# Kernel tuning notes

Hardware: AMD Instinct MI355X
Metric: run time of the kernel (lower is better)

The kernel has to match this reference:

```python
import jax, jax.numpy as jnp
import numpy as np

B, L, D = 32, 2048, 1024


def setup_inputs() -> dict:
    key = jax.random.key(0)
    ks = jax.random.split(key, 8)
    s = 1.0 / np.sqrt(D)
    s2 = 1.0 / np.sqrt(2 * D)
    return {
        "query": jax.random.normal(ks[0], (B, 1, D), dtype=jnp.float32),
        "context": jax.random.normal(ks[1], (B, L, D), dtype=jnp.float32),
        "W_in": jax.random.uniform(ks[2], (D, D), jnp.float32, -s, s),      # linear_in weight (no bias)
        "w_att": jax.random.uniform(ks[3], (2 * D,), jnp.float32, -s2, s2),  # nn.Linear(2D,1) weight, flattened
        "b_att": jax.random.uniform(ks[4], (1,), jnp.float32, -s2, s2),     # nn.Linear(2D,1) bias
        "W_out": jax.random.uniform(ks[5], (D, 2 * D), jnp.float32, -s2, s2),  # linear_out weight (no bias)
        "mask": jax.random.randint(ks[6], (B, L), 0, 2, dtype=jnp.int32),
    }


def reference(query, context, W_in, w_att, b_att, W_out, mask):
    # query: [B,1,D], context: [B,L,D], mask: [B,L]
    d = query.shape[-1]
    q = jnp.einsum('bd,ed->be', query[:, 0, :], W_in)  # linear_in: x @ W_in^T -> [B,D]
    # Additive score: tanh(Linear(cat([q_expanded, context])))
    # Split the [1, 2D] linear into query part and context part (no concat materialized).
    q_part = q @ w_att[:d]                               # [B]
    c_part = jnp.einsum('bld,d->bl', context, w_att[d:])  # [B,L]
    scores = jnp.tanh(q_part[:, None] + c_part + b_att[0])  # [B,L]
    scores = jnp.where(mask == 0, jnp.float32(-1e9), scores)
    weights = jax.nn.softmax(scores, axis=-1)            # [B,L]
    mix = jnp.einsum('bl,bld->bd', weights, context)     # [B,D]
    combined = jnp.concatenate([mix, q], axis=-1)        # [B,2D]
    output = jnp.tanh(combined @ W_out.T)[:, None, :]    # [B,1,D]
    return output, weights[:, None, :]
```

## Files before the change

### kernel.cpp

```cpp
#include <hip/hip_runtime.h>
#include <math.h>

#define B_DIM 32
#define L_DIM 2048
#define D_DIM 1024
#define NC    32
#define CHUNK (L_DIM / NC)
#define ROWS_PER_WAVE (CHUNK / 4)

__device__ __forceinline__ float wave_reduce_sum(float v) {
    #pragma unroll
    for (int off = 32; off > 0; off >>= 1)
        v += __shfl_xor(v, off, 64);
    return v;
}

__global__ __launch_bounds__(256) void k_linear_in(
        const float* __restrict__ query, const float* __restrict__ W_in,
        float* __restrict__ q_out) {
    const int wave = threadIdx.x >> 6;
    const int lane = threadIdx.x & 63;
    const int e = blockIdx.x * 4 + wave;
    const float4* W4 = (const float4*)(W_in + (size_t)e * D_DIM);
    float4 wrow[4];
    #pragma unroll
    for (int j = 0; j < 4; ++j) wrow[j] = W4[j * 64 + lane];
    for (int b = 0; b < B_DIM; ++b) {
        const float4* q4 = (const float4*)(query + (size_t)b * D_DIM);
        float local = 0.f;
        #pragma unroll
        for (int j = 0; j < 4; ++j) {
            float4 v = q4[j * 64 + lane];
            local += v.x * wrow[j].x + v.y * wrow[j].y
                   + v.z * wrow[j].z + v.w * wrow[j].w;
        }
        float s = wave_reduce_sum(local);
        if (lane == 0) q_out[(size_t)b * D_DIM + e] = s;
    }
}

__global__ __launch_bounds__(64) void k_spart(
        const float* __restrict__ q, const float* __restrict__ w_att,
        const float* __restrict__ b_att, float* __restrict__ spart) {
    const int b = blockIdx.x;
    const int lane = threadIdx.x;
    const float4* q4 = (const float4*)(q + (size_t)b * D_DIM);
    const float4* w4 = (const float4*)(w_att);
    float local = 0.f;
    #pragma unroll
    for (int j = 0; j < 4; ++j) {
        float4 a = q4[j * 64 + lane];
        float4 w = w4[j * 64 + lane];
        local += a.x * w.x + a.y * w.y + a.z * w.z + a.w * w.w;
    }
    float s = wave_reduce_sum(local);
    if (lane == 0) spart[b] = s + b_att[0];
}

__global__ __launch_bounds__(256) void k_scores(
        const float* __restrict__ context, const float* __restrict__ w_att,
        const int* __restrict__ mask, const float* __restrict__ spart,
        float* __restrict__ out_weights,
        float* __restrict__ pZ, float* __restrict__ pacc) {
    const int c = blockIdx.x;
    const int b = blockIdx.y;
    const int wave = threadIdx.x >> 6;
    const int lane = threadIdx.x & 63;

    float4 wc[4];
    const float4* w4 = (const float4*)(w_att + D_DIM);
    #pragma unroll
    for (int j = 0; j < 4; ++j) wc[j] = w4[j * 64 + lane];

    const float sp = spart[b];
    float4 acc[4];
    #pragma unroll
    for (int j = 0; j < 4; ++j) acc[j] = make_float4(0.f, 0.f, 0.f, 0.f);
    float z = 0.f;

    const int l0 = c * CHUNK;
    const float* ctx_b = context + (size_t)b * L_DIM * D_DIM;
    const int* mask_b = mask + (size_t)b * L_DIM;

    for (int r = 0; r < ROWS_PER_WAVE; ++r) {
        const int l = l0 + r * 4 + wave;
        const float4* row4 = (const float4*)(ctx_b + (size_t)l * D_DIM);
        float4 v[4];
        #pragma unroll
        for (int j = 0; j < 4; ++j) v[j] = row4[j * 64 + lane];
        float local = 0.f;
        #pragma unroll
        for (int j = 0; j < 4; ++j)
            local += v[j].x * wc[j].x + v[j].y * wc[j].y
                   + v[j].z * wc[j].z + v[j].w * wc[j].w;
        float s = wave_reduce_sum(local);
        float w = (mask_b[l] == 0) ? 0.f : expf(tanhf(sp + s));
        if (lane == 0) out_weights[(size_t)b * L_DIM + l] = w;
        z += w;
        #pragma unroll
        for (int j = 0; j < 4; ++j) {
            acc[j].x += w * v[j].x;
            acc[j].y += w * v[j].y;
            acc[j].z += w * v[j].z;
            acc[j].w += w * v[j].w;
        }
    }

    __shared__ float sacc[4][D_DIM];
    __shared__ float sz[4];
    #pragma unroll
    for (int j = 0; j < 4; ++j)
        ((float4*)sacc[wave])[j * 64 + lane] = acc[j];
    if (lane == 0) sz[wave] = z;
    __syncthreads();

    const int t = threadIdx.x;
    float4 s0 = ((const float4*)sacc[0])[t];
    float4 s1 = ((const float4*)sacc[1])[t];
    float4 s2 = ((const float4*)sacc[2])[t];
    float4 s3 = ((const float4*)sacc[3])[t];
    float4 tot;
    tot.x = s0.x + s1.x + s2.x + s3.x;
    tot.y = s0.y + s1.y + s2.y + s3.y;
    tot.z = s0.z + s1.z + s2.z + s3.z;
    tot.w = s0.w + s1.w + s2.w + s3.w;
    ((float4*)(pacc + ((size_t)(b * NC + c)) * D_DIM))[t] = tot;
    if (t == 0) pZ[b * NC + c] = sz[0] + sz[1] + sz[2] + sz[3];
}

__global__ __launch_bounds__(256) void k_reduce(
        const float* __restrict__ pacc, const float* __restrict__ pZ,
        float* __restrict__ mix, float* __restrict__ out_weights) {
    const int b = blockIdx.x;
    const int t = threadIdx.x;
    __shared__ float sInvZ;
    if (t == 0) {
        float zt = 0.f;
        for (int c = 0; c < NC; ++c) zt += pZ[b * NC + c];
        sInvZ = (zt > 0.f) ? 1.f / zt : 0.f;
    }
    __syncthreads();
    const float invZ = sInvZ;

    float4 tot = make_float4(0.f, 0.f, 0.f, 0.f);
    for (int c = 0; c < NC; ++c) {
        float4 v = ((const float4*)(pacc + ((size_t)(b * NC + c)) * D_DIM))[t];
        tot.x += v.x; tot.y += v.y; tot.z += v.z; tot.w += v.w;
    }
    tot.x *= invZ; tot.y *= invZ; tot.z *= invZ; tot.w *= invZ;
    ((float4*)(mix + (size_t)b * D_DIM))[t] = tot;

    #pragma unroll
    for (int i = 0; i < L_DIM / 256; ++i) {
        const size_t idx = (size_t)b * L_DIM + i * 256 + t;
        out_weights[idx] = out_weights[idx] * invZ;
    }
}

__global__ __launch_bounds__(256) void k_out(
        const float* __restrict__ mix, const float* __restrict__ q,
        const float* __restrict__ W_out, float* __restrict__ out) {
    const int wave = threadIdx.x >> 6;
    const int lane = threadIdx.x & 63;
    const int e = blockIdx.x * 4 + wave;
    const float4* W4 = (const float4*)(W_out + (size_t)e * (2 * D_DIM));
    float4 wrow[8];
    #pragma unroll
    for (int j = 0; j < 8; ++j) wrow[j] = W4[j * 64 + lane];
    for (int b = 0; b < B_DIM; ++b) {
        const float4* m4 = (const float4*)(mix + (size_t)b * D_DIM);
        const float4* q4 = (const float4*)(q + (size_t)b * D_DIM);
        float local = 0.f;
        #pragma unroll
        for (int j = 0; j < 4; ++j) {
            float4 v = m4[j * 64 + lane];
            local += v.x * wrow[j].x + v.y * wrow[j].y
                   + v.z * wrow[j].z + v.w * wrow[j].w;
        }
        #pragma unroll
        for (int j = 0; j < 4; ++j) {
            float4 v = q4[j * 64 + lane];
            local += v.x * wrow[j + 4].x + v.y * wrow[j + 4].y
                   + v.z * wrow[j + 4].z + v.w * wrow[j + 4].w;
        }
        float s = wave_reduce_sum(local);
        if (lane == 0) out[(size_t)b * D_DIM + e] = tanhf(s);
    }
}

extern "C" void kernel_launch(void* const* d_in, const int* in_sizes, int n_in,
                              void* d_out, int out_size, void* d_ws, size_t ws_size,
                              hipStream_t stream) {
    const float* query   = (const float*)d_in[0];
    const float* context = (const float*)d_in[1];
    const float* W_in    = (const float*)d_in[2];
    const float* w_att   = (const float*)d_in[3];
    const float* b_att   = (const float*)d_in[4];
    const float* W_out   = (const float*)d_in[5];
    const int*   mask    = (const int*)d_in[6];

    float* out   = (float*)d_out;
    float* out_w = out + (size_t)B_DIM * D_DIM;

    float* ws    = (float*)d_ws;
    float* q     = ws;
    float* spart = q + (size_t)B_DIM * D_DIM;
    float* pZ    = spart + B_DIM;
    float* pacc  = pZ + B_DIM * NC;
    float* mix   = pacc + (size_t)B_DIM * NC * D_DIM;

    k_linear_in<<<D_DIM / 4, 256, 0, stream>>>(query, W_in, q);
    k_spart<<<B_DIM, 64, 0, stream>>>(q, w_att, b_att, spart);
    k_scores<<<dim3(NC, B_DIM), 256, 0, stream>>>(context, w_att, mask, spart,
                                                  out_w, pZ, pacc);
    k_reduce<<<B_DIM, 256, 0, stream>>>(pacc, pZ, mix, out_w);
    k_out<<<D_DIM / 4, 256, 0, stream>>>(mix, q, W_out, out);
}
```

Measured before the change: 463.9 us.

## Prefetch next context row in score kernel and defer softmax normalization

The score kernel now loads the next context row into registers while it processes the current row, a software double-buffer meant to hide global memory latency. The reduce kernel sums the partial normalizers with a wave reduction, unrolls the chunk sum, and scales the weights with float4 accesses. It also writes the unnormalized mix plus a per-batch inverse normalizer, which the output GEMV applies to the mix dot product. The prefetch raises register pressure, and the context stream is the dominant cost.

```diff
diff --git a/kernel.cpp b/kernel.cpp
--- a/kernel.cpp
+++ b/kernel.cpp
@@ -82,12 +82,21 @@
     const float* ctx_b = context + (size_t)b * L_DIM * D_DIM;
     const int* mask_b = mask + (size_t)b * L_DIM;
 
+    float4 v[4];
+    {
+        const float4* row4 = (const float4*)(ctx_b + (size_t)(l0 + wave) * D_DIM);
+        #pragma unroll
+        for (int j = 0; j < 4; ++j) v[j] = row4[j * 64 + lane];
+    }
+
     for (int r = 0; r < ROWS_PER_WAVE; ++r) {
         const int l = l0 + r * 4 + wave;
-        const float4* row4 = (const float4*)(ctx_b + (size_t)l * D_DIM);
-        float4 v[4];
-        #pragma unroll
-        for (int j = 0; j < 4; ++j) v[j] = row4[j * 64 + lane];
+        float4 vn[4] = {};
+        if (r + 1 < ROWS_PER_WAVE) {
+            const float4* rn = (const float4*)(ctx_b + (size_t)(l + 4) * D_DIM);
+            #pragma unroll
+            for (int j = 0; j < 4; ++j) vn[j] = rn[j * 64 + lane];
+        }
         float local = 0.f;
         #pragma unroll
         for (int j = 0; j < 4; ++j)
@@ -104,6 +113,8 @@
             acc[j].z += w * v[j].z;
             acc[j].w += w * v[j].w;
         }
+        #pragma unroll
+        for (int j = 0; j < 4; ++j) v[j] = vn[j];
     }
 
     __shared__ float sacc[4][D_DIM];
@@ -130,36 +141,44 @@
 
 __global__ __launch_bounds__(256) void k_reduce(
         const float* __restrict__ pacc, const float* __restrict__ pZ,
-        float* __restrict__ mix, float* __restrict__ out_weights) {
+        float* __restrict__ mix_raw, float* __restrict__ invZ_out,
+        float* __restrict__ out_weights) {
     const int b = blockIdx.x;
     const int t = threadIdx.x;
     __shared__ float sInvZ;
-    if (t == 0) {
-        float zt = 0.f;
-        for (int c = 0; c < NC; ++c) zt += pZ[b * NC + c];
-        sInvZ = (zt > 0.f) ? 1.f / zt : 0.f;
+    if (t < 64) {
+        float zv = (t < NC) ? pZ[b * NC + t] : 0.f;
+        zv = wave_reduce_sum(zv);
+        if (t == 0) {
+            float inv = (zv > 0.f) ? 1.f / zv : 0.f;
+            sInvZ = inv;
+            invZ_out[b] = inv;
+        }
     }
     __syncthreads();
     const float invZ = sInvZ;
 
     float4 tot = make_float4(0.f, 0.f, 0.f, 0.f);
+    #pragma unroll 8
     for (int c = 0; c < NC; ++c) {
         float4 v = ((const float4*)(pacc + ((size_t)(b * NC + c)) * D_DIM))[t];
         tot.x += v.x; tot.y += v.y; tot.z += v.z; tot.w += v.w;
     }
-    tot.x *= invZ; tot.y *= invZ; tot.z *= invZ; tot.w *= invZ;
-    ((float4*)(mix + (size_t)b * D_DIM))[t] = tot;
-
-    #pragma unroll
-    for (int i = 0; i < L_DIM / 256; ++i) {
-        const size_t idx = (size_t)b * L_DIM + i * 256 + t;
-        out_weights[idx] = out_weights[idx] * invZ;
+    ((float4*)(mix_raw + (size_t)b * D_DIM))[t] = tot;
+
+    float4* w4 = (float4*)(out_weights + (size_t)b * L_DIM);
+    #pragma unroll
+    for (int i = 0; i < L_DIM / (256 * 4); ++i) {
+        float4 v = w4[i * 256 + t];
+        v.x *= invZ; v.y *= invZ; v.z *= invZ; v.w *= invZ;
+        w4[i * 256 + t] = v;
     }
 }
 
 __global__ __launch_bounds__(256) void k_out(
-        const float* __restrict__ mix, const float* __restrict__ q,
-        const float* __restrict__ W_out, float* __restrict__ out) {
+        const float* __restrict__ mix_raw, const float* __restrict__ q,
+        const float* __restrict__ invZ, const float* __restrict__ W_out,
+        float* __restrict__ out) {
     const int wave = threadIdx.x >> 6;
     const int lane = threadIdx.x & 63;
     const int e = blockIdx.x * 4 + wave;
@@ -168,22 +187,23 @@
     #pragma unroll
     for (int j = 0; j < 8; ++j) wrow[j] = W4[j * 64 + lane];
     for (int b = 0; b < B_DIM; ++b) {
-        const float4* m4 = (const float4*)(mix + (size_t)b * D_DIM);
+        const float4* m4 = (const float4*)(mix_raw + (size_t)b * D_DIM);
         const float4* q4 = (const float4*)(q + (size_t)b * D_DIM);
-        float local = 0.f;
+        const float iz = invZ[b];
+        float lmix = 0.f, lq = 0.f;
         #pragma unroll
         for (int j = 0; j < 4; ++j) {
             float4 v = m4[j * 64 + lane];
-            local += v.x * wrow[j].x + v.y * wrow[j].y
-                   + v.z * wrow[j].z + v.w * wrow[j].w;
+            lmix += v.x * wrow[j].x + v.y * wrow[j].y
+                  + v.z * wrow[j].z + v.w * wrow[j].w;
         }
         #pragma unroll
         for (int j = 0; j < 4; ++j) {
             float4 v = q4[j * 64 + lane];
-            local += v.x * wrow[j + 4].x + v.y * wrow[j + 4].y
-                   + v.z * wrow[j + 4].z + v.w * wrow[j + 4].w;
-        }
-        float s = wave_reduce_sum(local);
+            lq += v.x * wrow[j + 4].x + v.y * wrow[j + 4].y
+                + v.z * wrow[j + 4].z + v.w * wrow[j + 4].w;
+        }
+        float s = wave_reduce_sum(lmix * iz + lq);
         if (lane == 0) out[(size_t)b * D_DIM + e] = tanhf(s);
     }
 }
@@ -208,11 +228,12 @@
     float* pZ    = spart + B_DIM;
     float* pacc  = pZ + B_DIM * NC;
     float* mix   = pacc + (size_t)B_DIM * NC * D_DIM;
+    float* invZ  = mix + (size_t)B_DIM * D_DIM;
 
     k_linear_in<<<D_DIM / 4, 256, 0, stream>>>(query, W_in, q);
     k_spart<<<B_DIM, 64, 0, stream>>>(q, w_att, b_att, spart);
     k_scores<<<dim3(NC, B_DIM), 256, 0, stream>>>(context, w_att, mask, spart,
                                                   out_w, pZ, pacc);
-    k_reduce<<<B_DIM, 256, 0, stream>>>(pacc, pZ, mix, out_w);
-    k_out<<<D_DIM / 4, 256, 0, stream>>>(mix, q, W_out, out);
-}
+    k_reduce<<<B_DIM, 256, 0, stream>>>(pacc, pZ, mix, invZ, out_w);
+    k_out<<<D_DIM / 4, 256, 0, stream>>>(mix, q, invZ, W_out, out);
+}
```

After: 463.9 us. About the same (+0.0%).
